# Performance work log

Measured on AMD Instinct MI355X. Metric: run time of the kernel, lower is better.

Reference implementation:

```python
import jax, jax.numpy as jnp
import numpy as np

D_MODEL = 1024
H = 16
HEAD = D_MODEL // H  # 64


def setup_inputs() -> dict:
    key = jax.random.key(0)
    ks = jax.random.split(key, 10)
    B, S = 2, 2048
    x = jax.random.normal(ks[0], (B, S, D_MODEL), dtype=jnp.float32)
    y = jax.random.normal(ks[1], (B, S, D_MODEL), dtype=jnp.float32)
    mask = jnp.ones((B, S, S), dtype=jnp.float32)
    s = 1.0 / np.sqrt(D_MODEL)
    Wq = jax.random.normal(ks[2], (D_MODEL, D_MODEL), dtype=jnp.float32) * s
    Wk = jax.random.normal(ks[3], (D_MODEL, D_MODEL), dtype=jnp.float32) * s
    Wv = jax.random.normal(ks[4], (D_MODEL, D_MODEL), dtype=jnp.float32) * s
    Wo = jax.random.normal(ks[5], (D_MODEL, D_MODEL), dtype=jnp.float32) * s
    bq = jnp.zeros((D_MODEL,), jnp.float32)
    bk = jnp.zeros((D_MODEL,), jnp.float32)
    bv = jnp.zeros((D_MODEL,), jnp.float32)
    bo = jnp.zeros((D_MODEL,), jnp.float32)
    return {"x": x, "y": y, "mask": mask, "Wq": Wq, "bq": bq, "Wk": Wk,
            "bk": bk, "Wv": Wv, "bv": bv, "Wo": Wo, "bo": bo}


def reference(x, y, mask, Wq, bq, Wk, bk, Wv, bv, Wo, bo):
    # torch Linear: out = in @ W.T + b; here W stored as [out, in]
    B, Sq, D = x.shape
    Skv = y.shape[1]
    q = x @ Wq.T + bq  # [B, Sq, D]
    k = y @ Wk.T + bk  # [B, Skv, D]
    v = y @ Wv.T + bv
    # chunk(h, dim=-1) + cat(dim=0) == split feature dim into heads (head-major)
    q = q.reshape(B, Sq, H, HEAD)
    k = k.reshape(B, Skv, H, HEAD)
    v = v.reshape(B, Skv, H, HEAD)
    score = jnp.einsum('bqhd,bkhd->bhqk', q, k) / np.sqrt(HEAD)
    score = score + (1.0 - mask[:, None, :, :]) * -1e9
    attn = jax.nn.softmax(score, axis=-1)
    out = jnp.einsum('bhqk,bkhd->bqhd', attn, v).reshape(B, Sq, D)
    return out @ Wo.T + bo
```

## Files before the change

### kernel.cpp

```cpp
#include <hip/hip_runtime.h>
#include <cstdint>
#include <cstddef>

typedef __bf16 bf16x8 __attribute__((ext_vector_type(8)));
typedef float f32x4 __attribute__((ext_vector_type(4)));
typedef unsigned short u16;
typedef unsigned short u16x8 __attribute__((ext_vector_type(8)));
typedef unsigned int u32;

typedef __attribute__((address_space(1))) void gvoid_t;
typedef __attribute__((address_space(3))) void lvoid_t;

__device__ __forceinline__ void gld_lds16(const void* g, void* l) {
  __builtin_amdgcn_global_load_lds((gvoid_t*)g, (lvoid_t*)l, 16, 0, 0);
}

__device__ __forceinline__ u16 f2bf(float f) {
  u32 u = __float_as_uint(f);
  u += 0x7fffu + ((u >> 16) & 1u);
  return (u16)(u >> 16);
}
__device__ __forceinline__ u32 pack_rnd(float a, float b) {
  const u32 ua = __float_as_uint(a) + 0x8000u;
  const u32 ub = __float_as_uint(b) + 0x8000u;
  return __builtin_amdgcn_perm(ub, ua, 0x07060302u);
}
__device__ __forceinline__ bf16x8 ld_frag(const u16* p) {
  return __builtin_bit_cast(bf16x8, *(const uint4*)p);
}
__device__ __forceinline__ f32x4 mfma16(bf16x8 a, bf16x8 b, f32x4 c) {
  return __builtin_amdgcn_mfma_f32_16x16x32_bf16(a, b, c, 0, 0, 0);
}
__device__ __forceinline__ float ex2(float x) {
  return __builtin_amdgcn_exp2f(x);
}

#define D_MODEL 1024
#define SEQ     2048
#define NHEAD   16
#define QSC     0.1803368801f
#define MBIAS   (-1.4426950408e9f)

__global__ __launch_bounds__(256) void pre_kernel(
    const float* __restrict__ x,  const float* __restrict__ y,
    const float* __restrict__ wq, const float* __restrict__ wk,
    const float* __restrict__ wv, const float* __restrict__ wo,
    const float* __restrict__ mask,
    u16* __restrict__ xb, u16* __restrict__ yb,
    u16* __restrict__ wqb, u16* __restrict__ wkb,
    u16* __restrict__ wvb, u16* __restrict__ wob,
    u32* __restrict__ flags) {
  const int bid = blockIdx.x;
  if (bid >= 6144) {
    const int i = (((bid - 6144) * 256) + threadIdx.x) * 8;
    const float4 a = *(const float4*)(mask + i);
    const float4 b = *(const float4*)(mask + i + 4);
    const bool m8 = (a.x != 1.f) || (a.y != 1.f) || (a.z != 1.f) || (a.w != 1.f) ||
                    (b.x != 1.f) || (b.y != 1.f) || (b.z != 1.f) || (b.w != 1.f);
    const unsigned long long bal = __ballot(m8);
    const int lane = threadIdx.x & 63, wv8 = threadIdx.x >> 6;
    if (lane == 0) {
      u32 bits = 0;
#pragma unroll
      for (int g = 0; g < 8; ++g)
        bits |= (((bal >> (8 * g)) & 0xFFull) ? 1u : 0u) << g;
      if (bits) {
        const int row = bid - 6144;
        const int bb = row >> 11, q = row & 2047;
        atomicOr(&flags[bb * 32 + (q >> 6)], bits << (wv8 * 8));
      }
    }
    return;
  }
  const float* src;
  u16* dst;
  int base;
  float sA = 1.0f;
  if (bid < 2048)      { src = x;    dst = xb;    base = 0; }
  else if (bid < 4096) { src = y;    dst = yb;    base = 2048; }
  else if (bid < 4608) { src = wq;   dst = wqb;   base = 4096; sA = QSC; }
  else if (bid < 5120) { src = wk;   dst = wkb;   base = 4608; }
  else if (bid < 5632) { src = wv;   dst = wvb;   base = 5120; }
  else                 { src = wo;   dst = wob;   base = 5632; }
  const int i = (((bid - base) * 256) + threadIdx.x) * 8;
  const float4 a = *(const float4*)(src + i);
  const float4 b = *(const float4*)(src + i + 4);
  ushort4 lo, hi;
  lo.x = f2bf(a.x * sA); lo.y = f2bf(a.y * sA);
  lo.z = f2bf(a.z * sA); lo.w = f2bf(a.w * sA);
  hi.x = f2bf(b.x * sA); hi.y = f2bf(b.y * sA);
  hi.z = f2bf(b.z * sA); hi.w = f2bf(b.w * sA);
  *(ushort4*)(dst + i) = lo;
  *(ushort4*)(dst + i + 4) = hi;
}

template <int MODE, typename OT>
__device__ __forceinline__ void gemm_block_128(const u16* __restrict__ A,
                                               const u16* __restrict__ W,
                                               const float* __restrict__ bias,
                                               float bscale,
                                               OT* __restrict__ D,
                                               int mb, int nb) {
  __shared__ __align__(16) u16 S[16384];
  u16* Asl = S;
  u16* Bsl = S + 8192;
  const int tid = threadIdx.x;
  const int w = tid >> 6, lane = tid & 63, quad = lane >> 4, l16 = lane & 15;
  const int wm = (w & 1) * 64, wn = (w >> 1) * 64;
  const int cidx = w * 64 + lane;

  f32x4 acc[4][4];
#pragma unroll
  for (int i = 0; i < 4; ++i)
#pragma unroll
    for (int j = 0; j < 4; ++j) acc[i][j] = f32x4{0.f, 0.f, 0.f, 0.f};

  for (int k0 = 0; k0 < 1024; k0 += 64) {
    __syncthreads();
#pragma unroll
    for (int t = 0; t < 4; ++t) {
      const int idx = t * 256 + cidx;
      const int row = idx >> 3;
      const int g = (idx & 7) ^ (row & 7);
      const size_t dst = (size_t)(t * 4 + w) * 1024;
      gld_lds16(A + (size_t)(mb * 128 + row) * 1024 + k0 + g * 8, (char*)Asl + dst);
      gld_lds16(W + (size_t)(nb * 128 + row) * 1024 + k0 + g * 8, (char*)Bsl + dst);
    }
    __syncthreads();

#pragma unroll
    for (int kk = 0; kk < 2; ++kk) {
      bf16x8 af[4], bfr[4];
#pragma unroll
      for (int i = 0; i < 4; ++i) {
        const int ar = wm + i * 16 + l16;
        const int br = wn + i * 16 + l16;
        af[i]  = ld_frag(Asl + ar * 64 + (((kk * 4 + quad) ^ (ar & 7)) * 8));
        bfr[i] = ld_frag(Bsl + br * 64 + (((kk * 4 + quad) ^ (br & 7)) * 8));
      }
#pragma unroll
      for (int i = 0; i < 4; ++i)
#pragma unroll
        for (int j = 0; j < 4; ++j) acc[i][j] = mfma16(af[i], bfr[j], acc[i][j]);
    }
  }

  if constexpr (MODE == 2) {
    __syncthreads();
#pragma unroll
    for (int i = 0; i < 4; ++i)
#pragma unroll
      for (int j = 0; j < 4; ++j) {
        const int dl = wn + j * 16 + l16;
        const float bv = bias[nb * 128 + dl];
        const int sx = (wm + i * 16 + quad * 4) ^ ((dl & 15) << 3);
        uint2 pv;
        pv.x = (u32)f2bf(acc[i][j][0] + bv) | ((u32)f2bf(acc[i][j][1] + bv) << 16);
        pv.y = (u32)f2bf(acc[i][j][2] + bv) | ((u32)f2bf(acc[i][j][3] + bv) << 16);
        *(uint2*)(S + dl * 128 + sx) = pv;
      }
    __syncthreads();
    const int dl = tid >> 1, half = tid & 1;
    const int bb = mb >> 4, s0 = (mb & 15) * 128;
    u16* vrow = (u16*)D + (size_t)(bb * 1024 + nb * 128 + dl) * SEQ + s0 + half * 64;
#pragma unroll
    for (int c = 0; c < 8; ++c) {
      const int pc = (half * 8 + c) ^ (dl & 15);
      *(uint4*)(vrow + c * 8) = *(const uint4*)(S + dl * 128 + pc * 8);
    }
  } else {
#pragma unroll
    for (int i = 0; i < 4; ++i)
#pragma unroll
      for (int j = 0; j < 4; ++j) {
        const int gn = nb * 128 + wn + j * 16 + l16;
        const float bv = bias[gn] * bscale;
#pragma unroll
        for (int r = 0; r < 4; ++r) {
          const int gm = mb * 128 + wm + i * 16 + quad * 4 + r;
          const float v = acc[i][j][r] + bv;
          if constexpr (sizeof(OT) == 2)
            D[(size_t)gm * 1024 + gn] = (OT)f2bf(v);
          else
            D[(size_t)gm * 1024 + gn] = (OT)v;
        }
      }
  }
}

__device__ __forceinline__ void gemm_block_n64(const u16* __restrict__ A,
                                               const u16* __restrict__ W,
                                               const float* __restrict__ bias,
                                               float* __restrict__ D,
                                               int mb, int nb) {
  __shared__ __align__(16) u16 S[12288];
  u16* Asl = S;
  u16* Bsl = S + 8192;
  const int tid = threadIdx.x;
  const int w = tid >> 6, lane = tid & 63, quad = lane >> 4, l16 = lane & 15;
  const int wm = w * 32;
  const int cidx = w * 64 + lane;

  f32x4 acc[2][4];
#pragma unroll
  for (int i = 0; i < 2; ++i)
#pragma unroll
    for (int j = 0; j < 4; ++j) acc[i][j] = f32x4{0.f, 0.f, 0.f, 0.f};

  for (int k0 = 0; k0 < 1024; k0 += 64) {
    __syncthreads();
#pragma unroll
    for (int t = 0; t < 4; ++t) {
      const int idx = t * 256 + cidx;
      const int row = idx >> 3;
      const int g = (idx & 7) ^ (row & 7);
      gld_lds16(A + (size_t)(mb * 128 + row) * 1024 + k0 + g * 8,
                (char*)Asl + (size_t)(t * 4 + w) * 1024);
    }
#pragma unroll
    for (int t = 0; t < 2; ++t) {
      const int idx = t * 256 + cidx;
      const int row = idx >> 3;
      const int g = (idx & 7) ^ (row & 7);
      gld_lds16(W + (size_t)(nb * 64 + row) * 1024 + k0 + g * 8,
                (char*)Bsl + (size_t)(t * 4 + w) * 1024);
    }
    __syncthreads();

#pragma unroll
    for (int kk = 0; kk < 2; ++kk) {
      bf16x8 af[2], bfr[4];
#pragma unroll
      for (int i = 0; i < 2; ++i) {
        const int ar = wm + i * 16 + l16;
        af[i] = ld_frag(Asl + ar * 64 + (((kk * 4 + quad) ^ (ar & 7)) * 8));
      }
#pragma unroll
      for (int j = 0; j < 4; ++j) {
        const int br = j * 16 + l16;
        bfr[j] = ld_frag(Bsl + br * 64 + (((kk * 4 + quad) ^ (br & 7)) * 8));
      }
#pragma unroll
      for (int i = 0; i < 2; ++i)
#pragma unroll
        for (int j = 0; j < 4; ++j) acc[i][j] = mfma16(af[i], bfr[j], acc[i][j]);
    }
  }

#pragma unroll
  for (int i = 0; i < 2; ++i)
#pragma unroll
    for (int j = 0; j < 4; ++j) {
      const int gn = nb * 64 + j * 16 + l16;
      const float bv = bias[gn];
#pragma unroll
      for (int r = 0; r < 4; ++r) {
        const int gm = mb * 128 + wm + i * 16 + quad * 4 + r;
        D[(size_t)gm * 1024 + gn] = acc[i][j][r] + bv;
      }
    }
}

__global__ __launch_bounds__(256) void qkv_kernel(
    const u16* __restrict__ xb, const u16* __restrict__ yb,
    const u16* __restrict__ Wqb, const u16* __restrict__ Wkb, const u16* __restrict__ Wvb,
    const float* __restrict__ bq, const float* __restrict__ bk, const float* __restrict__ bv,
    u16* __restrict__ qb, u16* __restrict__ kb, u16* __restrict__ vt) {
  const int mat = blockIdx.y >> 3;
  const int nb = blockIdx.y & 7;
  const int mb = blockIdx.x;
  if (mat == 0)      gemm_block_128<0, u16>(xb, Wqb, bq, QSC,  qb, mb, nb);
  else if (mat == 1) gemm_block_128<0, u16>(yb, Wkb, bk, 1.0f, kb, mb, nb);
  else               gemm_block_128<2, u16>(yb, Wvb, bv, 1.0f, vt, mb, nb);
}

__global__ __launch_bounds__(256) void oproj_kernel(
    const u16* __restrict__ ctx, const u16* __restrict__ Wob,
    const float* __restrict__ bo, float* __restrict__ out) {
  gemm_block_n64(ctx, Wob, bo, out, blockIdx.x, blockIdx.y);
}

__global__ __launch_bounds__(256) void attn_kernel(
    const u16* __restrict__ qb, const u16* __restrict__ kb,
    const u16* __restrict__ vt, const float* __restrict__ mask,
    const u32* __restrict__ flags, u16* __restrict__ ctx) {
  const int h = blockIdx.x;
  const int qblk = blockIdx.y;
  const int b = blockIdx.z;
  const int tid = threadIdx.x, w = tid >> 6, lane = tid & 63;
  const int quad = lane >> 4, l16 = lane & 15;
  const int q0 = qblk * 64;

  __shared__ __align__(16) u16 Ks[64 * 64];
  __shared__ __align__(16) u16 Vs[64 * 64];
  __shared__ __align__(16) u16 Ps[64 * 64];

  const u32 fl = flags[(b << 5) + qblk];

  const int qrow = w * 16 + l16;
  const u16* qp = qb + (size_t)(b * SEQ + q0 + qrow) * D_MODEL + h * 64;
  const bf16x8 qf0 = ld_frag(qp + quad * 8);
  const bf16x8 qf1 = ld_frag(qp + 32 + quad * 8);

  bf16x8 onesf;
  {
    u16x8 t;
    const u16 ov = (l16 == 0) ? (u16)0x3F80 : (u16)0;
#pragma unroll
    for (int j = 0; j < 8; ++j) t[j] = ov;
    onesf = __builtin_bit_cast(bf16x8, t);
  }

  f32x4 O[4];
#pragma unroll
  for (int dt = 0; dt < 4; ++dt) O[dt] = f32x4{0.f, 0.f, 0.f, 0.f};
  f32x4 O4 = f32x4{0.f, 0.f, 0.f, 0.f};

  const int cidx = w * 64 + lane;
  const int bhalf = (quad & 1) * 4;

  const int r0 = cidx >> 3,        g0 = (cidx & 7) ^ (r0 & 7);
  const int r1 = (256 + cidx) >> 3, g1 = ((256 + cidx) & 7) ^ (r1 & 7);
  const u16* kp0 = kb + (size_t)(b * SEQ + r0) * D_MODEL + h * 64 + g0 * 8;
  const u16* kp1 = kb + (size_t)(b * SEQ + r1) * D_MODEL + h * 64 + g1 * 8;
  const u16* vp0 = vt + ((size_t)((b * NHEAD + h) * 64 + r0)) * SEQ + g0 * 8;
  const u16* vp1 = vt + ((size_t)((b * NHEAD + h) * 64 + r1)) * SEQ + g1 * 8;
  const float* mp = mask + (size_t)(b * SEQ + q0 + qrow) * SEQ + quad * 4;
  const size_t dst0 = (size_t)w * 1024;
  const size_t dst1 = (size_t)(4 + w) * 1024;

  for (int kt = 0; kt < 32; ++kt) {
    const bool doBias = (fl >> kt) & 1u;
    __syncthreads();
    gld_lds16(kp0, (char*)Ks + dst0);
    gld_lds16(kp1, (char*)Ks + dst1);
    gld_lds16(vp0, (char*)Vs + dst0);
    gld_lds16(vp1, (char*)Vs + dst1);
    kp0 += 64 * D_MODEL; kp1 += 64 * D_MODEL;
    vp0 += 64;           vp1 += 64;
    __syncthreads();

    f32x4 z[4];
    __builtin_amdgcn_s_setprio(1);
#pragma unroll
    for (int nt = 0; nt < 4; ++nt) {
      const int kvl = nt * 16 + l16;
      const bf16x8 kf0 = ld_frag(Ks + kvl * 64 + ((quad ^ (kvl & 7)) * 8));
      const bf16x8 kf1 = ld_frag(Ks + kvl * 64 + (((4 + quad) ^ (kvl & 7)) * 8));
      f32x4 zz;
      if (doBias) {
        const float4 mv = *(const float4*)(mp + nt * 16);
        zz[0] = (1.f - mv.x) * MBIAS;
        zz[1] = (1.f - mv.y) * MBIAS;
        zz[2] = (1.f - mv.z) * MBIAS;
        zz[3] = (1.f - mv.w) * MBIAS;
      } else {
        zz = f32x4{0.f, 0.f, 0.f, 0.f};
      }
      zz = mfma16(kf0, qf0, zz);
      zz = mfma16(kf1, qf1, zz);
      z[nt] = zz;
    }
    __builtin_amdgcn_s_setprio(0);
    mp += 64;
#pragma unroll
    for (int nt = 0; nt < 4; ++nt) {
      uint2 pv;
      pv.x = pack_rnd(ex2(z[nt][0]), ex2(z[nt][1]));
      pv.y = pack_rnd(ex2(z[nt][2]), ex2(z[nt][3]));
      const int ck = nt * 2 + (quad >> 1);
      *(uint2*)(Ps + qrow * 64 + ((ck ^ (qrow & 7)) * 8) + bhalf) = pv;
    }

    const bf16x8 pf0 = ld_frag(Ps + qrow * 64 + ((quad ^ (qrow & 7)) * 8));
    const bf16x8 pf1 = ld_frag(Ps + qrow * 64 + (((4 + quad) ^ (qrow & 7)) * 8));
    __builtin_amdgcn_s_setprio(1);
#pragma unroll
    for (int dt = 0; dt < 4; ++dt) {
      const int vr = dt * 16 + l16;
      const bf16x8 vf0 = ld_frag(Vs + vr * 64 + ((quad ^ (vr & 7)) * 8));
      const bf16x8 vf1 = ld_frag(Vs + vr * 64 + (((4 + quad) ^ (vr & 7)) * 8));
      O[dt] = mfma16(pf0, vf0, O[dt]);
      O[dt] = mfma16(pf1, vf1, O[dt]);
    }
    O4 = mfma16(pf0, onesf, O4);
    O4 = mfma16(pf1, onesf, O4);
    __builtin_amdgcn_s_setprio(0);
  }

  float inv[4];
#pragma unroll
  for (int r = 0; r < 4; ++r)
    inv[r] = 1.0f / __shfl(O4[r], lane & 48, 64);

#pragma unroll
  for (int dt = 0; dt < 4; ++dt)
#pragma unroll
    for (int r = 0; r < 4; ++r) {
      const int gq = b * SEQ + q0 + w * 16 + quad * 4 + r;
      const int gd = h * 64 + dt * 16 + l16;
      ctx[(size_t)gq * D_MODEL + gd] = f2bf(O[dt][r] * inv[r]);
    }
}

extern "C" void kernel_launch(void* const* d_in, const int* in_sizes, int n_in,
                              void* d_out, int out_size, void* d_ws, size_t ws_size,
                              hipStream_t stream) {
  (void)in_sizes; (void)n_in; (void)out_size; (void)ws_size;
  const float* x    = (const float*)d_in[0];
  const float* y    = (const float*)d_in[1];
  const float* mask = (const float*)d_in[2];
  const float* Wq   = (const float*)d_in[3];
  const float* bq   = (const float*)d_in[4];
  const float* Wk   = (const float*)d_in[5];
  const float* bk   = (const float*)d_in[6];
  const float* Wv   = (const float*)d_in[7];
  const float* bv   = (const float*)d_in[8];
  const float* Wo   = (const float*)d_in[9];
  const float* bo   = (const float*)d_in[10];
  float* out = (float*)d_out;

  const size_t M4 = (size_t)4096 * 1024;
  const size_t M1 = (size_t)1024 * 1024;
  u16* qbuf  = (u16*)d_ws;
  u16* kbuf  = qbuf + M4;
  u16* vt    = kbuf + M4;
  u16* cbuf  = vt + M4;
  u16* wob   = cbuf + M4;
  u16* xb    = wob + M1;
  u16* yb    = xb + M4;
  u16* wqb   = yb + M4;
  u16* wkb   = wqb + M1;
  u16* wvb   = wkb + M1;
  u32* flags = (u32*)(wvb + M1);

  hipMemsetAsync(flags, 0, 64 * sizeof(u32), stream);
  pre_kernel<<<dim3(10240, 1, 1), 256, 0, stream>>>(
      x, y, Wq, Wk, Wv, Wo, mask, xb, yb, wqb, wkb, wvb, wob, flags);
  qkv_kernel<<<dim3(32, 24, 1), 256, 0, stream>>>(xb, yb, wqb, wkb, wvb,
                                                  bq, bk, bv, qbuf, kbuf, vt);
  attn_kernel<<<dim3(NHEAD, 32, 2), 256, 0, stream>>>(qbuf, kbuf, vt, mask, flags, cbuf);
  oproj_kernel<<<dim3(32, 16, 1), 256, 0, stream>>>(cbuf, wob, bo, out);
}
```

Baseline: 244.0 us.

## Move mask scan and Wo conversion into QKV kernel; hoist attention LDS addresses

Moves the mask-flag scan and the Wo fp32-to-bf16 conversion out of the preprocessing kernel and into extra blocks of the QKV projection kernel, so that memory-bound work can overlap with GEMM blocks. The mask blocks now each loop over 32 rows instead of handling one row per block. Separately, the attention kernel precomputes its swizzled LDS fragment addresses outside the key loop and adds a launch-bounds occupancy hint of 4 blocks. The trade-off is more register pressure from the hoisted pointers, and mask-scan blocks that run much longer than the others inside the QKV grid.

```diff
diff --git a/kernel.cpp b/kernel.cpp
--- a/kernel.cpp
+++ b/kernel.cpp
@@ -44,34 +44,11 @@
 __global__ __launch_bounds__(256) void pre_kernel(
     const float* __restrict__ x,  const float* __restrict__ y,
     const float* __restrict__ wq, const float* __restrict__ wk,
-    const float* __restrict__ wv, const float* __restrict__ wo,
-    const float* __restrict__ mask,
+    const float* __restrict__ wv,
     u16* __restrict__ xb, u16* __restrict__ yb,
     u16* __restrict__ wqb, u16* __restrict__ wkb,
-    u16* __restrict__ wvb, u16* __restrict__ wob,
-    u32* __restrict__ flags) {
+    u16* __restrict__ wvb) {
   const int bid = blockIdx.x;
-  if (bid >= 6144) {
-    const int i = (((bid - 6144) * 256) + threadIdx.x) * 8;
-    const float4 a = *(const float4*)(mask + i);
-    const float4 b = *(const float4*)(mask + i + 4);
-    const bool m8 = (a.x != 1.f) || (a.y != 1.f) || (a.z != 1.f) || (a.w != 1.f) ||
-                    (b.x != 1.f) || (b.y != 1.f) || (b.z != 1.f) || (b.w != 1.f);
-    const unsigned long long bal = __ballot(m8);
-    const int lane = threadIdx.x & 63, wv8 = threadIdx.x >> 6;
-    if (lane == 0) {
-      u32 bits = 0;
-#pragma unroll
-      for (int g = 0; g < 8; ++g)
-        bits |= (((bal >> (8 * g)) & 0xFFull) ? 1u : 0u) << g;
-      if (bits) {
-        const int row = bid - 6144;
-        const int bb = row >> 11, q = row & 2047;
-        atomicOr(&flags[bb * 32 + (q >> 6)], bits << (wv8 * 8));
-      }
-    }
-    return;
-  }
   const float* src;
   u16* dst;
   int base;
@@ -80,8 +57,7 @@
   else if (bid < 4096) { src = y;    dst = yb;    base = 2048; }
   else if (bid < 4608) { src = wq;   dst = wqb;   base = 4096; sA = QSC; }
   else if (bid < 5120) { src = wk;   dst = wkb;   base = 4608; }
-  else if (bid < 5632) { src = wv;   dst = wvb;   base = 5120; }
-  else                 { src = wo;   dst = wob;   base = 5632; }
+  else                 { src = wv;   dst = wvb;   base = 5120; }
   const int i = (((bid - base) * 256) + threadIdx.x) * 8;
   const float4 a = *(const float4*)(src + i);
   const float4 b = *(const float4*)(src + i + 4);
@@ -265,9 +241,48 @@
     const u16* __restrict__ xb, const u16* __restrict__ yb,
     const u16* __restrict__ Wqb, const u16* __restrict__ Wkb, const u16* __restrict__ Wvb,
     const float* __restrict__ bq, const float* __restrict__ bk, const float* __restrict__ bv,
-    u16* __restrict__ qb, u16* __restrict__ kb, u16* __restrict__ vt) {
-  const int mat = blockIdx.y >> 3;
-  const int nb = blockIdx.y & 7;
+    const float* __restrict__ mask, const float* __restrict__ wo,
+    u16* __restrict__ qb, u16* __restrict__ kb, u16* __restrict__ vt,
+    u16* __restrict__ wob, u32* __restrict__ flags) {
+  const int by = blockIdx.y;
+  if (by < 4) {
+    const int mx = by * 32 + blockIdx.x;
+    const int lane = threadIdx.x & 63, wv8 = threadIdx.x >> 6;
+    for (int r = 0; r < 32; ++r) {
+      const int row = mx * 32 + r;
+      const size_t i = (size_t)row * SEQ + threadIdx.x * 8;
+      const float4 a = *(const float4*)(mask + i);
+      const float4 b = *(const float4*)(mask + i + 4);
+      const bool m8 = (a.x != 1.f) || (a.y != 1.f) || (a.z != 1.f) || (a.w != 1.f) ||
+                      (b.x != 1.f) || (b.y != 1.f) || (b.z != 1.f) || (b.w != 1.f);
+      const unsigned long long bal = __ballot(m8);
+      if (lane == 0) {
+        u32 bits = 0;
+#pragma unroll
+        for (int g = 0; g < 8; ++g)
+          bits |= (((bal >> (8 * g)) & 0xFFull) ? 1u : 0u) << g;
+        if (bits) {
+          const int bb = row >> 11, q = row & 2047;
+          atomicOr(&flags[bb * 32 + (q >> 6)], bits << (wv8 * 8));
+        }
+      }
+    }
+    return;
+  }
+  if (by < 20) {
+    const int wid = (by - 4) * 32 + blockIdx.x;
+    const int i = (wid * 256 + threadIdx.x) * 8;
+    const float4 a = *(const float4*)(wo + i);
+    const float4 b = *(const float4*)(wo + i + 4);
+    ushort4 lo, hi;
+    lo.x = f2bf(a.x); lo.y = f2bf(a.y); lo.z = f2bf(a.z); lo.w = f2bf(a.w);
+    hi.x = f2bf(b.x); hi.y = f2bf(b.y); hi.z = f2bf(b.z); hi.w = f2bf(b.w);
+    *(ushort4*)(wob + i) = lo;
+    *(ushort4*)(wob + i + 4) = hi;
+    return;
+  }
+  const int mat = (by - 20) >> 3;
+  const int nb = (by - 20) & 7;
   const int mb = blockIdx.x;
   if (mat == 0)      gemm_block_128<0, u16>(xb, Wqb, bq, QSC,  qb, mb, nb);
   else if (mat == 1) gemm_block_128<0, u16>(yb, Wkb, bk, 1.0f, kb, mb, nb);
@@ -280,7 +295,7 @@
   gemm_block_n64(ctx, Wob, bo, out, blockIdx.x, blockIdx.y);
 }
 
-__global__ __launch_bounds__(256) void attn_kernel(
+__global__ __launch_bounds__(256, 4) void attn_kernel(
     const u16* __restrict__ qb, const u16* __restrict__ kb,
     const u16* __restrict__ vt, const float* __restrict__ mask,
     const u32* __restrict__ flags, u16* __restrict__ ctx) {
@@ -319,6 +334,21 @@
   const int cidx = w * 64 + lane;
   const int bhalf = (quad & 1) * 4;
 
+  const u16 *kf0p[4], *kf1p[4], *vf0p[4], *vf1p[4];
+  u16* psp[4];
+#pragma unroll
+  for (int nt = 0; nt < 4; ++nt) {
+    const int rl = nt * 16 + l16;
+    kf0p[nt] = Ks + rl * 64 + ((quad ^ (rl & 7)) * 8);
+    kf1p[nt] = Ks + rl * 64 + (((4 + quad) ^ (rl & 7)) * 8);
+    vf0p[nt] = Vs + rl * 64 + ((quad ^ (rl & 7)) * 8);
+    vf1p[nt] = Vs + rl * 64 + (((4 + quad) ^ (rl & 7)) * 8);
+    const int ck = nt * 2 + (quad >> 1);
+    psp[nt] = Ps + qrow * 64 + ((ck ^ (qrow & 7)) * 8) + bhalf;
+  }
+  const u16* pf0p = Ps + qrow * 64 + ((quad ^ (qrow & 7)) * 8);
+  const u16* pf1p = Ps + qrow * 64 + (((4 + quad) ^ (qrow & 7)) * 8);
+
   const int r0 = cidx >> 3,        g0 = (cidx & 7) ^ (r0 & 7);
   const int r1 = (256 + cidx) >> 3, g1 = ((256 + cidx) & 7) ^ (r1 & 7);
   const u16* kp0 = kb + (size_t)(b * SEQ + r0) * D_MODEL + h * 64 + g0 * 8;
@@ -344,9 +374,8 @@
     __builtin_amdgcn_s_setprio(1);
 #pragma unroll
     for (int nt = 0; nt < 4; ++nt) {
-      const int kvl = nt * 16 + l16;
-      const bf16x8 kf0 = ld_frag(Ks + kvl * 64 + ((quad ^ (kvl & 7)) * 8));
-      const bf16x8 kf1 = ld_frag(Ks + kvl * 64 + (((4 + quad) ^ (kvl & 7)) * 8));
+      const bf16x8 kf0 = ld_frag(kf0p[nt]);
+      const bf16x8 kf1 = ld_frag(kf1p[nt]);
       f32x4 zz;
       if (doBias) {
         const float4 mv = *(const float4*)(mp + nt * 16);
@@ -368,18 +397,16 @@
       uint2 pv;
       pv.x = pack_rnd(ex2(z[nt][0]), ex2(z[nt][1]));
       pv.y = pack_rnd(ex2(z[nt][2]), ex2(z[nt][3]));
-      const int ck = nt * 2 + (quad >> 1);
-      *(uint2*)(Ps + qrow * 64 + ((ck ^ (qrow & 7)) * 8) + bhalf) = pv;
-    }
-
-    const bf16x8 pf0 = ld_frag(Ps + qrow * 64 + ((quad ^ (qrow & 7)) * 8));
-    const bf16x8 pf1 = ld_frag(Ps + qrow * 64 + (((4 + quad) ^ (qrow & 7)) * 8));
+      *(uint2*)psp[nt] = pv;
+    }
+
+    const bf16x8 pf0 = ld_frag(pf0p);
+    const bf16x8 pf1 = ld_frag(pf1p);
     __builtin_amdgcn_s_setprio(1);
 #pragma unroll
     for (int dt = 0; dt < 4; ++dt) {
-      const int vr = dt * 16 + l16;
-      const bf16x8 vf0 = ld_frag(Vs + vr * 64 + ((quad ^ (vr & 7)) * 8));
-      const bf16x8 vf1 = ld_frag(Vs + vr * 64 + (((4 + quad) ^ (vr & 7)) * 8));
+      const bf16x8 vf0 = ld_frag(vf0p[dt]);
+      const bf16x8 vf1 = ld_frag(vf1p[dt]);
       O[dt] = mfma16(pf0, vf0, O[dt]);
       O[dt] = mfma16(pf1, vf1, O[dt]);
     }
@@ -435,10 +462,11 @@
   u32* flags = (u32*)(wvb + M1);
 
   hipMemsetAsync(flags, 0, 64 * sizeof(u32), stream);
-  pre_kernel<<<dim3(10240, 1, 1), 256, 0, stream>>>(
-      x, y, Wq, Wk, Wv, Wo, mask, xb, yb, wqb, wkb, wvb, wob, flags);
-  qkv_kernel<<<dim3(32, 24, 1), 256, 0, stream>>>(xb, yb, wqb, wkb, wvb,
-                                                  bq, bk, bv, qbuf, kbuf, vt);
+  pre_kernel<<<dim3(5632, 1, 1), 256, 0, stream>>>(
+      x, y, Wq, Wk, Wv, xb, yb, wqb, wkb, wvb);
+  qkv_kernel<<<dim3(32, 44, 1), 256, 0, stream>>>(xb, yb, wqb, wkb, wvb,
+                                                  bq, bk, bv, mask, Wo,
+                                                  qbuf, kbuf, vt, wob, flags);
   attn_kernel<<<dim3(NHEAD, 32, 2), 256, 0, stream>>>(qbuf, kbuf, vt, mask, flags, cbuf);
   oproj_kernel<<<dim3(32, 16, 1), 256, 0, stream>>>(cbuf, wob, bo, out);
 }
```

Measured after the change: 240.1 us. About the same (-1.6%).
